# Kernel tuning notes

Hardware: AMD Instinct MI355X
Metric: run time of the kernel (lower is better)

The kernel has to match this reference:

```python
import jax, jax.numpy as jnp
import numpy as np

B, F, D = 4096, 39, 16
L0, L1 = 128, 128
H1 = L0 // 2  # split_half: half the maps feed the next layer


def setup_inputs() -> dict:
    key = jax.random.key(0)
    k0, k1, k2, k3, k4 = jax.random.split(key, 5)
    x = jax.random.normal(k0, (B, F, D), dtype=jnp.float32)
    # Conv1D(size, 1, channels_first) == matmul over channel dim: W [out, in]
    W0 = jax.random.normal(k1, (L0, F * F), dtype=jnp.float32) * 0.02
    b0 = jnp.zeros((L0,), dtype=jnp.float32)
    W1 = jax.random.normal(k2, (L1, H1 * F), dtype=jnp.float32) * 0.02
    b1 = jnp.zeros((L1,), dtype=jnp.float32)
    return {"x": x, "W0": W0, "b0": b0, "W1": W1, "b1": b1}


def _cin_layer(h, h0, W, b):
    # h: [B, H, D], h0: [B, F, D] -> outer product [B, H*F, D], then 1x1 conv
    z = jnp.einsum('bhd,bmd->bhmd', h, h0)
    z = z.reshape(z.shape[0], -1, z.shape[-1])          # [B, H*F, D]
    y = jnp.einsum('oc,bcd->bod', W, z) + b[None, :, None]
    return jax.nn.relu(y)


def reference(x, W0, b0, W1, b1):
    h0 = x
    # layer 0 (split_half, not last): split into next_hidden / direct_connect
    y0 = _cin_layer(h0, h0, W0, b0)                     # [B, L0, D]
    next_hidden, direct0 = y0[:, :H1, :], y0[:, H1:, :]
    # layer 1 (last): all maps are direct connect
    direct1 = _cin_layer(next_hidden, h0, W1, b1)       # [B, L1, D]
    result = jnp.sum(jnp.concatenate([direct0, direct1], axis=1), axis=-1)
    return result  # [B, L0//2 + L1]
```

## Files before the change

### kernel.cpp

```cpp
#include <hip/hip_runtime.h>
#include <hip/hip_fp16.h>

#define B_    4096
#define F_    39
#define D_    16
#define NKK0  50
#define NKK1  80
#define NKK   130
#define NRND  65
#define WP_HALFS (NKK * 4096)

typedef _Float16 f16x8  __attribute__((ext_vector_type(8)));
typedef float    f32x4  __attribute__((ext_vector_type(4)));
typedef float    f32x16 __attribute__((ext_vector_type(16)));

union FragAB { f16x8 h8; __half2 h2[4]; f32x4 f4; __half h[8]; };

__device__ __forceinline__ void gload_lds16(const void* g, void* l) {
    __builtin_amdgcn_global_load_lds(
        (const __attribute__((address_space(1))) void*)g,
        (__attribute__((address_space(3))) void*)l, 16, 0, 0);
}

__global__ __launch_bounds__(256) void prep_w(
    const float* __restrict__ W0, const float* __restrict__ W1,
    __half* __restrict__ Wp)
{
    int idx = blockIdx.x * 256 + threadIdx.x;
    if (idx >= WP_HALFS) return;
    int j   = idx & 7;
    int l   = (idx >> 3) & 63;
    int ks  = (idx >> 9) & 1;
    int Mt  = (idx >> 10) & 3;
    int kkg = idx >> 12;
    int o   = Mt * 32 + (l & 31);
    int sub = l >> 5;
    float v = 0.f;
    if (kkg < NKK0) {
        int u = 4 * kkg + 2 * ks + sub;
        int a = u / 40, h = u - 40 * a, m = a * 8 + j;
        if (h < F_ && m < F_) v = W0[o * (F_ * F_) + h * F_ + m];
    } else {
        int u = 4 * (kkg - NKK0) + 2 * ks + sub;
        int a = u >> 6, h = u & 63, m = a * 8 + j;
        if (m < F_) v = W1[o * (64 * F_) + h * F_ + m];
    }
    Wp[idx] = __float2half(v);
}

template<int LL, int AA>
__device__ __forceinline__ void do_round(
    int rr, int t, int sub,
    const __half* xrowA, const __half* xrowB,
    const __half* nrowA, const __half* nrowB,
    const FragAB (&xmc)[2][5], f32x16 (&acc)[2][2],
    __half* WlFlat, int wl_thread,
    int& buf, int& rg, const __half*& wsrc)
{
    if (rg < NRND - 1) {
        __half* dst = WlFlat + (buf ^ 1) * 8192;
#pragma unroll
        for (int it = 0; it < 4; ++it)
            gload_lds16(wsrc + it * 2048 + t * 8, dst + it * 2048 + t * 8);
        wsrc += 8192;
    }
    const __half* wl  = WlFlat + buf * 8192 + wl_thread;
    const __half* hbA = LL ? nrowA : xrowA;
    const __half* hbB = LL ? nrowB : xrowB;

#pragma unroll
    for (int kk2 = 0; kk2 < 2; ++kk2) {
#pragma unroll
        for (int ks = 0; ks < 2; ++ks) {
            const int hoff = 8 * rr + 4 * kk2 + 2 * ks + sub;
            __half2 xa2 = __half2half2(hbA[hoff]);
            __half2 xb2 = __half2half2(hbB[hoff]);
            FragAB bA, bB;
#pragma unroll
            for (int q = 0; q < 4; ++q) {
                bA.h2[q] = __hmul2(xmc[0][AA].h2[q], xa2);
                bB.h2[q] = __hmul2(xmc[1][AA].h2[q], xb2);
            }
#pragma unroll
            for (int mt = 0; mt < 2; ++mt) {
                FragAB A;
                A.f4 = *(const f32x4*)(wl + kk2 * 4096 + mt * 1024 + ks * 512);
                acc[mt][0] = __builtin_amdgcn_mfma_f32_32x32x16_f16(
                    A.h8, bA.h8, acc[mt][0], 0, 0, 0);
                acc[mt][1] = __builtin_amdgcn_mfma_f32_32x32x16_f16(
                    A.h8, bB.h8, acc[mt][1], 0, 0, 0);
            }
        }
    }
    asm volatile("s_waitcnt vmcnt(0)" ::: "memory");
    __syncthreads();
    buf ^= 1; ++rg;
}

__global__ __launch_bounds__(256, 2) void cin_main(
    const float* __restrict__ x, const float* __restrict__ b0,
    const float* __restrict__ b1, const __half* __restrict__ Wp,
    float* __restrict__ out)
{
    __shared__ __align__(16) __half Wl[2][8192];
    __shared__ __align__(16) __half xT[8][16][40];
    __shared__ __align__(16) __half nhT[8][16][68];

    const int t    = threadIdx.x;
    const int w    = t >> 6, lane = t & 63;
    const int sub  = lane >> 5, bp = (lane >> 4) & 1, d = lane & 15;
    const int g    = w >> 1, hi = w & 1;
    const int gb   = blockIdx.x * 8;

#pragma unroll
    for (int it = 0; it < 4; ++it)
        gload_lds16(Wp + it * 2048 + t * 8, &Wl[0][0] + it * 2048 + t * 8);

    for (int i = t; i < 8 * 156; i += 256) {
        int bt = i / 156, r2 = i - bt * 156;
        int f = r2 >> 2, dq = r2 & 3;
        const float4 v = *(const float4*)&x[((size_t)(gb + bt) * F_ + f) * D_ + dq * 4];
        xT[bt][dq * 4 + 0][f] = __float2half(v.x);
        xT[bt][dq * 4 + 1][f] = __float2half(v.y);
        xT[bt][dq * 4 + 2][f] = __float2half(v.z);
        xT[bt][dq * 4 + 3][f] = __float2half(v.w);
    }
    if (t < 128) xT[t >> 4][t & 15][39] = __float2half(0.f);

    asm volatile("s_waitcnt vmcnt(0)" ::: "memory");
    __syncthreads();

    const int btA = g * 4 + bp;
    const int btB = g * 4 + 2 + bp;
    const __half* xrowA = &xT[btA][d][0];
    const __half* xrowB = &xT[btB][d][0];
    const __half* nrowA = &nhT[btA][d][0];
    const __half* nrowB = &nhT[btB][d][0];
    FragAB xmc[2][5];
#pragma unroll
    for (int a = 0; a < 5; ++a) {
        xmc[0][a].f4 = *(const f32x4*)(xrowA + a * 8);
        xmc[1][a].f4 = *(const f32x4*)(xrowB + a * 8);
    }

    f32x16 acc[2][2];
#pragma unroll
    for (int mt = 0; mt < 2; ++mt) {
        const int Mt = hi * 2 + mt;
#pragma unroll
        for (int r = 0; r < 16; ++r) {
            float bv = b0[Mt * 32 + (r & 3) + 8 * (r >> 2) + 4 * sub];
            acc[mt][0][r] = bv; acc[mt][1][r] = bv;
        }
    }

    const int wl_thread = (hi * 2) * 1024 + lane * 8;
    __half* WlFlat = &Wl[0][0];
    int buf = 0, rg = 0;
    const __half* wsrc = Wp + 8192;

#pragma unroll 1
    for (int rr = 0; rr < 5; ++rr) do_round<0,0>(rr,t,sub,xrowA,xrowB,nrowA,nrowB,xmc,acc,WlFlat,wl_thread,buf,rg,wsrc);
#pragma unroll 1
    for (int rr = 0; rr < 5; ++rr) do_round<0,1>(rr,t,sub,xrowA,xrowB,nrowA,nrowB,xmc,acc,WlFlat,wl_thread,buf,rg,wsrc);
#pragma unroll 1
    for (int rr = 0; rr < 5; ++rr) do_round<0,2>(rr,t,sub,xrowA,xrowB,nrowA,nrowB,xmc,acc,WlFlat,wl_thread,buf,rg,wsrc);
#pragma unroll 1
    for (int rr = 0; rr < 5; ++rr) do_round<0,3>(rr,t,sub,xrowA,xrowB,nrowA,nrowB,xmc,acc,WlFlat,wl_thread,buf,rg,wsrc);
#pragma unroll 1
    for (int rr = 0; rr < 5; ++rr) do_round<0,4>(rr,t,sub,xrowA,xrowB,nrowA,nrowB,xmc,acc,WlFlat,wl_thread,buf,rg,wsrc);

    if (hi) {
#pragma unroll
        for (int mt = 0; mt < 2; ++mt) {
            const int Mt = 2 + mt;
#pragma unroll
            for (int p = 0; p < 2; ++p) {
#pragma unroll
                for (int r = 0; r < 16; ++r) {
                    float v = fmaxf(acc[mt][p][r], 0.f);
                    v += __shfl_xor(v, 1); v += __shfl_xor(v, 2);
                    v += __shfl_xor(v, 4); v += __shfl_xor(v, 8);
                    if (d == 0) {
                        int row = Mt * 32 + (r & 3) + 8 * (r >> 2) + 4 * sub;
                        int b   = gb + g * 4 + p * 2 + bp;
                        out[(size_t)b * 192 + (row - 64)] = v;
                    }
                }
            }
        }
    } else {
#pragma unroll
        for (int mt = 0; mt < 2; ++mt) {
#pragma unroll
            for (int p = 0; p < 2; ++p) {
                __half* nr = (__half*)(p ? nrowB : nrowA);
#pragma unroll
                for (int rg4 = 0; rg4 < 4; ++rg4) {
                    union { __half h[4]; float2 f2; } pk;
#pragma unroll
                    for (int q = 0; q < 4; ++q)
                        pk.h[q] = __float2half(fmaxf(acc[mt][p][rg4 * 4 + q], 0.f));
                    int row0 = mt * 32 + 8 * rg4 + 4 * sub;
                    *(float2*)(nr + row0) = pk.f2;
                }
            }
        }
    }
#pragma unroll
    for (int mt = 0; mt < 2; ++mt) {
        const int Mt = hi * 2 + mt;
#pragma unroll
        for (int r = 0; r < 16; ++r) {
            float bv = b1[Mt * 32 + (r & 3) + 8 * (r >> 2) + 4 * sub];
            acc[mt][0][r] = bv; acc[mt][1][r] = bv;
        }
    }
    __syncthreads();

#pragma unroll 1
    for (int rr = 0; rr < 8; ++rr) do_round<1,0>(rr,t,sub,xrowA,xrowB,nrowA,nrowB,xmc,acc,WlFlat,wl_thread,buf,rg,wsrc);
#pragma unroll 1
    for (int rr = 0; rr < 8; ++rr) do_round<1,1>(rr,t,sub,xrowA,xrowB,nrowA,nrowB,xmc,acc,WlFlat,wl_thread,buf,rg,wsrc);
#pragma unroll 1
    for (int rr = 0; rr < 8; ++rr) do_round<1,2>(rr,t,sub,xrowA,xrowB,nrowA,nrowB,xmc,acc,WlFlat,wl_thread,buf,rg,wsrc);
#pragma unroll 1
    for (int rr = 0; rr < 8; ++rr) do_round<1,3>(rr,t,sub,xrowA,xrowB,nrowA,nrowB,xmc,acc,WlFlat,wl_thread,buf,rg,wsrc);
#pragma unroll 1
    for (int rr = 0; rr < 8; ++rr) do_round<1,4>(rr,t,sub,xrowA,xrowB,nrowA,nrowB,xmc,acc,WlFlat,wl_thread,buf,rg,wsrc);

#pragma unroll
    for (int mt = 0; mt < 2; ++mt) {
        const int Mt = hi * 2 + mt;
#pragma unroll
        for (int p = 0; p < 2; ++p) {
#pragma unroll
            for (int r = 0; r < 16; ++r) {
                float v = fmaxf(acc[mt][p][r], 0.f);
                v += __shfl_xor(v, 1); v += __shfl_xor(v, 2);
                v += __shfl_xor(v, 4); v += __shfl_xor(v, 8);
                if (d == 0) {
                    int row = Mt * 32 + (r & 3) + 8 * (r >> 2) + 4 * sub;
                    int b   = gb + g * 4 + p * 2 + bp;
                    out[(size_t)b * 192 + 64 + row] = v;
                }
            }
        }
    }
}

extern "C" void kernel_launch(void* const* d_in, const int* in_sizes, int n_in,
                              void* d_out, int out_size, void* d_ws, size_t ws_size,
                              hipStream_t stream) {
    const float* x  = (const float*)d_in[0];
    const float* W0 = (const float*)d_in[1];
    const float* b0 = (const float*)d_in[2];
    const float* W1 = (const float*)d_in[3];
    const float* b1 = (const float*)d_in[4];
    float* out = (float*)d_out;
    __half* Wp = (__half*)d_ws;

    prep_w<<<(WP_HALFS + 255) / 256, 256, 0, stream>>>(W0, W1, Wp);
    cin_main<<<B_ / 8, 256, 0, stream>>>(x, b0, b1, Wp, out);
}
```

Baseline: 87.89 us.

## Triple-buffer weight tiles with one barrier per round and partial vmcnt waits

Moves the weight staging in shared memory from a double buffer to a triple buffer. Each round now prefetches two rounds ahead, waits only for the older loads with vmcnt(4), and uses a single barrier at the start of the round instead of a full drain plus syncthreads at the end. This lets global-to-LDS loads overlap MFMA work for longer. Biases are also cached in shared memory. The cost is 16 KB more LDS per block, which could lower occupancy, plus some redundant clamped loads on the final rounds. The interaction between the initial x global loads, the vmcnt counts and the lgkmcnt barrier needs care to stay correct.

```diff
diff --git a/kernel.cpp b/kernel.cpp
--- a/kernel.cpp
+++ b/kernel.cpp
@@ -55,16 +55,23 @@
     const __half* nrowA, const __half* nrowB,
     const FragAB (&xmc)[2][5], f32x16 (&acc)[2][2],
     __half* WlFlat, int wl_thread,
-    int& buf, int& rg, const __half*& wsrc)
+    int& rd, int& rg, const __half* __restrict__ Wp)
 {
-    if (rg < NRND - 1) {
-        __half* dst = WlFlat + (buf ^ 1) * 8192;
+    asm volatile("s_waitcnt vmcnt(4)" ::: "memory");
+    __builtin_amdgcn_s_barrier();
+    asm volatile("" ::: "memory");
+
+    {
+        int sb = rd + 2; if (sb >= 3) sb -= 3;
+        int rs = rg + 2; if (rs > NRND - 1) rs = NRND - 1;
+        __half* dst = WlFlat + sb * 8192;
+        const __half* src = Wp + (size_t)rs * 8192;
 #pragma unroll
         for (int it = 0; it < 4; ++it)
-            gload_lds16(wsrc + it * 2048 + t * 8, dst + it * 2048 + t * 8);
-        wsrc += 8192;
-    }
-    const __half* wl  = WlFlat + buf * 8192 + wl_thread;
+            gload_lds16(src + it * 2048 + t * 8, dst + it * 2048 + t * 8);
+    }
+
+    const __half* wl  = WlFlat + rd * 8192 + wl_thread;
     const __half* hbA = LL ? nrowA : xrowA;
     const __half* hbB = LL ? nrowB : xrowB;
 
@@ -92,9 +99,8 @@
             }
         }
     }
-    asm volatile("s_waitcnt vmcnt(0)" ::: "memory");
-    __syncthreads();
-    buf ^= 1; ++rg;
+    rd = (rd + 1 == 3) ? 0 : (rd + 1);
+    ++rg;
 }
 
 __global__ __launch_bounds__(256, 2) void cin_main(
@@ -102,9 +108,10 @@
     const float* __restrict__ b1, const __half* __restrict__ Wp,
     float* __restrict__ out)
 {
-    __shared__ __align__(16) __half Wl[2][8192];
+    __shared__ __align__(16) __half Wl[3][8192];
     __shared__ __align__(16) __half xT[8][16][40];
     __shared__ __align__(16) __half nhT[8][16][68];
+    __shared__ float bs0[128], bs1[128];
 
     const int t    = threadIdx.x;
     const int w    = t >> 6, lane = t & 63;
@@ -112,9 +119,7 @@
     const int g    = w >> 1, hi = w & 1;
     const int gb   = blockIdx.x * 8;
 
-#pragma unroll
-    for (int it = 0; it < 4; ++it)
-        gload_lds16(Wp + it * 2048 + t * 8, &Wl[0][0] + it * 2048 + t * 8);
+    if (t < 128) { bs0[t] = b0[t]; bs1[t] = b1[t]; }
 
     for (int i = t; i < 8 * 156; i += 256) {
         int bt = i / 156, r2 = i - bt * 156;
@@ -127,8 +132,17 @@
     }
     if (t < 128) xT[t >> 4][t & 15][39] = __float2half(0.f);
 
-    asm volatile("s_waitcnt vmcnt(0)" ::: "memory");
-    __syncthreads();
+    __half* WlFlat = &Wl[0][0];
+#pragma unroll
+    for (int r0 = 0; r0 < 2; ++r0)
+#pragma unroll
+        for (int it = 0; it < 4; ++it)
+            gload_lds16(Wp + (size_t)r0 * 8192 + it * 2048 + t * 8,
+                        WlFlat + r0 * 8192 + it * 2048 + t * 8);
+
+    asm volatile("s_waitcnt lgkmcnt(0)" ::: "memory");
+    __builtin_amdgcn_s_barrier();
+    asm volatile("" ::: "memory");
 
     const int btA = g * 4 + bp;
     const int btB = g * 4 + 2 + bp;
@@ -149,26 +163,24 @@
         const int Mt = hi * 2 + mt;
 #pragma unroll
         for (int r = 0; r < 16; ++r) {
-            float bv = b0[Mt * 32 + (r & 3) + 8 * (r >> 2) + 4 * sub];
+            float bv = bs0[Mt * 32 + (r & 3) + 8 * (r >> 2) + 4 * sub];
             acc[mt][0][r] = bv; acc[mt][1][r] = bv;
         }
     }
 
     const int wl_thread = (hi * 2) * 1024 + lane * 8;
-    __half* WlFlat = &Wl[0][0];
-    int buf = 0, rg = 0;
-    const __half* wsrc = Wp + 8192;
-
-#pragma unroll 1
-    for (int rr = 0; rr < 5; ++rr) do_round<0,0>(rr,t,sub,xrowA,xrowB,nrowA,nrowB,xmc,acc,WlFlat,wl_thread,buf,rg,wsrc);
-#pragma unroll 1
-    for (int rr = 0; rr < 5; ++rr) do_round<0,1>(rr,t,sub,xrowA,xrowB,nrowA,nrowB,xmc,acc,WlFlat,wl_thread,buf,rg,wsrc);
-#pragma unroll 1
-    for (int rr = 0; rr < 5; ++rr) do_round<0,2>(rr,t,sub,xrowA,xrowB,nrowA,nrowB,xmc,acc,WlFlat,wl_thread,buf,rg,wsrc);
-#pragma unroll 1
-    for (int rr = 0; rr < 5; ++rr) do_round<0,3>(rr,t,sub,xrowA,xrowB,nrowA,nrowB,xmc,acc,WlFlat,wl_thread,buf,rg,wsrc);
-#pragma unroll 1
-    for (int rr = 0; rr < 5; ++rr) do_round<0,4>(rr,t,sub,xrowA,xrowB,nrowA,nrowB,xmc,acc,WlFlat,wl_thread,buf,rg,wsrc);
+    int rd = 0, rg = 0;
+
+#pragma unroll 1
+    for (int rr = 0; rr < 5; ++rr) do_round<0,0>(rr,t,sub,xrowA,xrowB,nrowA,nrowB,xmc,acc,WlFlat,wl_thread,rd,rg,Wp);
+#pragma unroll 1
+    for (int rr = 0; rr < 5; ++rr) do_round<0,1>(rr,t,sub,xrowA,xrowB,nrowA,nrowB,xmc,acc,WlFlat,wl_thread,rd,rg,Wp);
+#pragma unroll 1
+    for (int rr = 0; rr < 5; ++rr) do_round<0,2>(rr,t,sub,xrowA,xrowB,nrowA,nrowB,xmc,acc,WlFlat,wl_thread,rd,rg,Wp);
+#pragma unroll 1
+    for (int rr = 0; rr < 5; ++rr) do_round<0,3>(rr,t,sub,xrowA,xrowB,nrowA,nrowB,xmc,acc,WlFlat,wl_thread,rd,rg,Wp);
+#pragma unroll 1
+    for (int rr = 0; rr < 5; ++rr) do_round<0,4>(rr,t,sub,xrowA,xrowB,nrowA,nrowB,xmc,acc,WlFlat,wl_thread,rd,rg,Wp);
 
     if (hi) {
 #pragma unroll
@@ -212,22 +224,24 @@
         const int Mt = hi * 2 + mt;
 #pragma unroll
         for (int r = 0; r < 16; ++r) {
-            float bv = b1[Mt * 32 + (r & 3) + 8 * (r >> 2) + 4 * sub];
+            float bv = bs1[Mt * 32 + (r & 3) + 8 * (r >> 2) + 4 * sub];
             acc[mt][0][r] = bv; acc[mt][1][r] = bv;
         }
     }
-    __syncthreads();
-
-#pragma unroll 1
-    for (int rr = 0; rr < 8; ++rr) do_round<1,0>(rr,t,sub,xrowA,xrowB,nrowA,nrowB,xmc,acc,WlFlat,wl_thread,buf,rg,wsrc);
-#pragma unroll 1
-    for (int rr = 0; rr < 8; ++rr) do_round<1,1>(rr,t,sub,xrowA,xrowB,nrowA,nrowB,xmc,acc,WlFlat,wl_thread,buf,rg,wsrc);
-#pragma unroll 1
-    for (int rr = 0; rr < 8; ++rr) do_round<1,2>(rr,t,sub,xrowA,xrowB,nrowA,nrowB,xmc,acc,WlFlat,wl_thread,buf,rg,wsrc);
-#pragma unroll 1
-    for (int rr = 0; rr < 8; ++rr) do_round<1,3>(rr,t,sub,xrowA,xrowB,nrowA,nrowB,xmc,acc,WlFlat,wl_thread,buf,rg,wsrc);
-#pragma unroll 1
-    for (int rr = 0; rr < 8; ++rr) do_round<1,4>(rr,t,sub,xrowA,xrowB,nrowA,nrowB,xmc,acc,WlFlat,wl_thread,buf,rg,wsrc);
+    asm volatile("s_waitcnt lgkmcnt(0)" ::: "memory");
+    __builtin_amdgcn_s_barrier();
+    asm volatile("" ::: "memory");
+
+#pragma unroll 1
+    for (int rr = 0; rr < 8; ++rr) do_round<1,0>(rr,t,sub,xrowA,xrowB,nrowA,nrowB,xmc,acc,WlFlat,wl_thread,rd,rg,Wp);
+#pragma unroll 1
+    for (int rr = 0; rr < 8; ++rr) do_round<1,1>(rr,t,sub,xrowA,xrowB,nrowA,nrowB,xmc,acc,WlFlat,wl_thread,rd,rg,Wp);
+#pragma unroll 1
+    for (int rr = 0; rr < 8; ++rr) do_round<1,2>(rr,t,sub,xrowA,xrowB,nrowA,nrowB,xmc,acc,WlFlat,wl_thread,rd,rg,Wp);
+#pragma unroll 1
+    for (int rr = 0; rr < 8; ++rr) do_round<1,3>(rr,t,sub,xrowA,xrowB,nrowA,nrowB,xmc,acc,WlFlat,wl_thread,rd,rg,Wp);
+#pragma unroll 1
+    for (int rr = 0; rr < 8; ++rr) do_round<1,4>(rr,t,sub,xrowA,xrowB,nrowA,nrowB,xmc,acc,WlFlat,wl_thread,rd,rg,Wp);
 
 #pragma unroll
     for (int mt = 0; mt < 2; ++mt) {
```

New measurement: 88.51 us. No clear change (+0.7%).
